# Optimization experiments

Hardware: AMD Instinct MI355X
Metric: run time of the kernel (lower is better)

## Reference

```python
import jax, jax.numpy as jnp
import numpy as np

B, T, H, Dk = 2, 2048, 8, 64
D = H * Dk
MAX_TIMESCALE = 10000.0
MIN_TIMESCALE = 2.0


def sinusoid_position_encoding(seq_len, hidden):
    # Non-causal symmetric relative positions: length 2*seq_len.
    freqs = np.arange(0, hidden, MIN_TIMESCALE)
    inv_freq = MAX_TIMESCALE ** (-freqs / hidden)
    pos_seq = np.arange(seq_len, -seq_len, -1.0)  # [2T]
    sinusoid = np.einsum('i,j->ij', pos_seq, inv_freq)  # [2T, hidden/2]
    pe = np.concatenate([np.sin(sinusoid), np.cos(sinusoid)], axis=-1)
    return jnp.asarray(pe, dtype=jnp.float32)  # [2T, hidden]


def rel_shift(logits):
    # Transformer-XL shift (general, non-causal): [b,h,t,2t] -> [b,h,t,t]
    b, h, t, total = logits.shape  # total == 2t
    x = logits.reshape(b, h, total, t)[:, :, 1:, :]
    x = x.reshape(b, h, t, total - 1)
    return x[..., :t]


def setup_inputs() -> dict:
    key = jax.random.key(0)
    ks = jax.random.split(key, 14)
    s = 1.0 / np.sqrt(D).astype(np.float32)  # VarianceScaling(1.0)-like
    return {
        'query': jax.random.normal(ks[0], (B, T, D), jnp.float32),
        'key_in': jax.random.normal(ks[1], (B, T, D), jnp.float32),
        'value': jax.random.normal(ks[2], (B, T, D), jnp.float32),
        'Wq': jax.random.normal(ks[3], (D, H * Dk), jnp.float32) * s,
        'bq': jnp.zeros((H * Dk,), jnp.float32),
        'Wk': jax.random.normal(ks[4], (D, H * Dk), jnp.float32) * s,
        'bk': jnp.zeros((H * Dk,), jnp.float32),
        'Wv': jax.random.normal(ks[5], (D, H * Dk), jnp.float32) * s,
        'bv': jnp.zeros((H * Dk,), jnp.float32),
        'Wr': jax.random.normal(ks[6], (D, D), jnp.float32) * s,
        'content_bias': jax.random.normal(ks[7], (H, Dk), jnp.float32) * 0.02,
        'relative_bias': jax.random.normal(ks[8], (H, Dk), jnp.float32) * 0.02,
        'Wo': jax.random.normal(ks[9], (H * Dk, D), jnp.float32) * s,
        'bo': jnp.zeros((D,), jnp.float32),
    }


def reference(query, key_in, value, Wq, bq, Wk, bk, Wv, bv, Wr,
              content_bias, relative_bias, Wo, bo):
    q = (query @ Wq + bq).reshape(B, T, H, Dk)
    k = (key_in @ Wk + bk).reshape(B, T, H, Dk)
    v = (value @ Wv + bv).reshape(B, T, H, Dk)

    # Content logits with learned per-head content bias.
    content_logits = jnp.einsum('bthd,bThd->bhtT', q + content_bias, k)

    # Relative-position keys: sinusoid encodings projected (no bias).
    pos = sinusoid_position_encoding(T, D)          # [2T, D]
    rel_k = (pos @ Wr).reshape(2 * T, H, Dk)        # [2T, H, Dk]
    relative_logits = jnp.einsum('bthd,Thd->bhtT', q + relative_bias, rel_k)
    relative_logits = rel_shift(relative_logits)    # [B,H,T,T]

    attn_logits = (content_logits + relative_logits) / np.sqrt(Dk).astype(np.float32)
    attn_weights = jax.nn.softmax(attn_logits)      # [B,H,T,T]

    attn = jnp.einsum('bhtT,bThd->bthd', attn_weights, v)
    attn_vec = attn.reshape(B, T, H * Dk)
    return attn_vec @ Wo + bo
```

## Files before the change

kernel.cpp:

```cpp
#include <hip/hip_runtime.h>
#include <math.h>

#define BB 2
#define TT 2048
#define HH 8
#define DK 64
#define DD 512
#define MM (BB * TT)
#define WSZ (128 * 4096)

typedef unsigned int u32;
typedef unsigned short u16;
typedef __bf16 bf16x8 __attribute__((ext_vector_type(8)));
typedef float f32x4 __attribute__((ext_vector_type(4)));

union frag_u { bf16x8 f; u16 u[8]; u32 w[4]; };

__device__ __forceinline__ void split2(float x, u16& h, u16& l) {
    u32 u = __float_as_uint(x);
    u32 hi = (u + 0x7fffu + ((u >> 16) & 1u)) >> 16;
    float hif = __uint_as_float(hi << 16);
    float lof = x - hif;
    u32 ul = __float_as_uint(lof);
    u32 lo = (ul + 0x7fffu + ((ul >> 16) & 1u)) >> 16;
    h = (u16)hi; l = (u16)lo;
}
__device__ __forceinline__ u32 split_pack(float x) {
    u16 h, l; split2(x, h, l);
    return ((u32)h << 16) | (u32)l;
}
__device__ __forceinline__ u16 bf16_rne(float x) {
    u32 u = __float_as_uint(x);
    return (u16)((u + 0x7fffu + ((u >> 16) & 1u)) >> 16);
}

__device__ __forceinline__ void load_lds16(const void* g, void* l) {
    __builtin_amdgcn_global_load_lds(
        (const __attribute__((address_space(1))) void*)g,
        (__attribute__((address_space(3))) void*)l, 16, 0, 0);
}

__device__ __forceinline__ void pack_granule(const float* xs, u16* dt, int g) {
    u32 hw[4], lw[4];
#pragma unroll
    for (int e = 0; e < 4; e++) {
        u16 h0, l0, h1, l1;
        split2(xs[2 * e], h0, l0);
        split2(xs[2 * e + 1], h1, l1);
        hw[e] = (u32)h0 | ((u32)h1 << 16);
        lw[e] = (u32)l0 | ((u32)l1 << 16);
    }
    *(uint4*)(dt + g * 8)        = make_uint4(hw[0], hw[1], hw[2], hw[3]);
    *(uint4*)(dt + 2048 + g * 8) = make_uint4(lw[0], lw[1], lw[2], lw[3]);
}

__device__ __forceinline__ void prepack_a_body(
    const float* __restrict__ src, u16* __restrict__ dst, int bid, int tid) {
    const int r = tid >> 3, f = tid & 7;
    const float* p = src + ((size_t)(bid >> 3) * 32 + r) * 512
                         + (size_t)(bid & 7) * 64 + f * 8;
    float4 a  = *(const float4*)p;
    float4 b4 = *(const float4*)(p + 4);
    float xs[8] = {a.x, a.y, a.z, a.w, b4.x, b4.y, b4.z, b4.w};
    const int s = f >> 2, kq = f & 3, nt = r >> 4, n = r & 15;
    const int g = nt * 128 + n * 8 + ((4 * s + kq + 5 * n) & 7);
    pack_granule(xs, dst + (size_t)bid * 4096, g);
}

__global__ __launch_bounds__(256) void prepack_all_kernel(
    const float* __restrict__ W0, const float* __restrict__ W1,
    const float* __restrict__ W2, const float* __restrict__ W3,
    const float* __restrict__ W4, u16* __restrict__ dstW,
    u16* __restrict__ dstPe,
    const float* __restrict__ sq, const float* __restrict__ sk,
    const float* __restrict__ sv, u16* __restrict__ dq,
    u16* __restrict__ dk, u16* __restrict__ dv) {
    __shared__ float tw[64][36];
    const int tid = threadIdx.x;
    if (blockIdx.x < 640) {
        const int bid = blockIdx.x;
        const int widx = bid >> 7, loc = bid & 127;
        const int nb2 = loc >> 3, kb = loc & 7;
        const float* Wsrc = widx == 0 ? W0 : widx == 1 ? W1 : widx == 2 ? W2
                          : widx == 3 ? W3 : W4;
        const int kl = tid >> 2, gr = tid & 3;
        const float* p = Wsrc + (size_t)(kb * 64 + kl) * 512 + nb2 * 32 + gr * 8;
        float4 a  = *(const float4*)p;
        float4 b4 = *(const float4*)(p + 4);
        *(float4*)&tw[kl][gr * 8]     = a;
        *(float4*)&tw[kl][gr * 8 + 4] = b4;
        __syncthreads();
        const int n5 = tid >> 3, f = tid & 7, s = f >> 2, kq = f & 3;
        float xs[8];
#pragma unroll
        for (int e = 0; e < 8; e++) xs[e] = tw[s * 32 + kq * 8 + e][n5];
        const int n = n5 & 15, nt = n5 >> 4;
        const int g = nt * 128 + n * 8 + ((4 * s + kq + 5 * n) & 7);
        pack_granule(xs, dstW + (size_t)bid * 4096, g);
    } else if (blockIdx.x < 1664) {
        const int bid = blockIdx.x - 640;
        const int r = tid >> 3, f = tid & 7;
        const int m  = (bid >> 3) * 32 + r;
        const int c0 = (bid & 7) * 64 + f * 8;
        float xs[8];
#pragma unroll
        for (int e = 0; e < 8; e++) {
            int col = c0 + e;
            int j = col & 255;
            double inv_freq = exp((double)(-2 * j) * (9.210340371976184 / 512.0));
            double ang = (double)(TT - m) * inv_freq;
            xs[e] = (col < 256) ? (float)sin(ang) : (float)cos(ang);
        }
        const int s = f >> 2, kq = f & 3, nt = r >> 4, n = r & 15;
        const int g = nt * 128 + n * 8 + ((4 * s + kq + 5 * n) & 7);
        pack_granule(xs, dstPe + (size_t)bid * 4096, g);
    } else {
        const int bid = blockIdx.x - 1664;
        const int sel = bid >> 10, sub = bid & 1023;
        const float* s = sel == 0 ? sq : sel == 1 ? sk : sv;
        u16* d = sel == 0 ? dq : sel == 1 ? dk : dv;
        prepack_a_body(s, d, sub, tid);
    }
}

__device__ __forceinline__ void gemm_full(
    const u16* __restrict__ Apk, const u16* __restrict__ Wpk,
    const float* __restrict__ bias, float* __restrict__ C,
    u16* __restrict__ Ppk, const float* __restrict__ dotv,
    float* __restrict__ dotout, int EPI, int bx, int tid) {
    __shared__ __align__(16) u16 Stage[2][16384];

    const int w = tid >> 6, lane = tid & 63, quad = lane >> 4, c = lane & 15;
    const int mp = bx & 63, nb = bx >> 6;
    const int mq = w >> 1, nq = w & 1;

    auto stage_async = [&](int kb, int half) {
        const u16* s = (w < 2)
            ? Apk + (size_t)((2 * mp + w) * 8 + kb) * 4096
            : Wpk + (size_t)((2 * nb + (w & 1)) * 8 + kb) * 4096;
        const u16* g = s + lane * 8;
        u16* d = Stage[half] + w * 4096;
#pragma unroll
        for (int u2 = 0; u2 < 8; u2++)
            load_lds16(g + u2 * 512, d + u2 * 512);
    };

    stage_async(0, 0);

    f32x4 acc[2][2];
#pragma unroll
    for (int mh = 0; mh < 2; mh++)
#pragma unroll
        for (int nh = 0; nh < 2; nh++) acc[mh][nh] = (f32x4){0.f, 0.f, 0.f, 0.f};

    for (int kb = 0; kb < 8; kb++) {
        const int half = kb & 1;
        __syncthreads();
        if (kb < 7) stage_async(kb + 1, 1 - half);
        const u16* Ab = Stage[half] + mq * 4096;
        const u16* Wb = Stage[half] + 8192 + nq * 4096;
#pragma unroll
        for (int s = 0; s < 2; s++) {
            bf16x8 ah[2], al[2], wh[2], wl[2];
#pragma unroll
            for (int t = 0; t < 2; t++) {
                int g = (t << 7) + (c << 3) + (((s << 2) + quad + 5 * c) & 7);
                ah[t] = *(const bf16x8*)(Ab + g * 8);
                al[t] = *(const bf16x8*)(Ab + 2048 + g * 8);
                wh[t] = *(const bf16x8*)(Wb + g * 8);
                wl[t] = *(const bf16x8*)(Wb + 2048 + g * 8);
            }
#pragma unroll
            for (int mh = 0; mh < 2; mh++)
#pragma unroll
                for (int nh = 0; nh < 2; nh++) {
                    acc[mh][nh] = __builtin_amdgcn_mfma_f32_16x16x32_bf16(
                        ah[mh], wh[nh], acc[mh][nh], 0, 0, 0);
                    acc[mh][nh] = __builtin_amdgcn_mfma_f32_16x16x32_bf16(
                        ah[mh], wl[nh], acc[mh][nh], 0, 0, 0);
                    acc[mh][nh] = __builtin_amdgcn_mfma_f32_16x16x32_bf16(
                        al[mh], wh[nh], acc[mh][nh], 0, 0, 0);
                }
        }
    }

    const int n0 = nb * 64 + nq * 32;
    float bv0 = bias ? bias[n0 + c] : 0.f;
    float bv1 = bias ? bias[n0 + 16 + c] : 0.f;

    if (EPI == 0) {
        const int m0 = mp * 64 + mq * 32;
#pragma unroll
        for (int mh = 0; mh < 2; mh++)
#pragma unroll
            for (int r = 0; r < 4; r++) {
                size_t row = (size_t)(m0 + mh * 16 + quad * 4 + r) * 512;
                C[row + n0 + c]      = acc[mh][0][r] + bv0;
                C[row + n0 + 16 + c] = acc[mh][1][r] + bv1;
            }
        return;
    }

    __syncthreads();
    float (*Cl)[68] = (float (*)[68])Stage;
    {
        const int rbase = mq * 32;
#pragma unroll
        for (int mh = 0; mh < 2; mh++)
#pragma unroll
            for (int r = 0; r < 4; r++) {
                int row = rbase + mh * 16 + quad * 4 + r;
                Cl[row][nq * 32 + c]      = acc[mh][0][r] + bv0;
                Cl[row][nq * 32 + 16 + c] = acc[mh][1][r] + bv1;
            }
    }
    __syncthreads();

    if (EPI == 2) {
        const int b = mp >> 5, jt0 = (mp & 31) * 2;
        const int d = tid >> 2, kq = tid & 3;
        const int n = d & 15;
        const int g = (d >> 4) * 64 + n * 4 + ((kq + (n >> 1)) & 3);
#pragma unroll
        for (int ht = 0; ht < 2; ht++) {
            float xs[8];
#pragma unroll
            for (int e = 0; e < 8; e++) xs[e] = Cl[ht * 32 + kq * 8 + e][d];
            u16* dt = Ppk + (size_t)(b * 512 + nb * 64 + jt0 + ht) * 4096;
            pack_granule(xs, dt, g);
        }
        return;
    }

    {
        const float scl = (EPI == 4) ? 1.0f : 0.125f;
        const int rr = tid >> 3, f = tid & 7;
        const int s = f >> 2, kq = f & 3, nt = rr >> 4, n = rr & 15;
        const int g = nt * 128 + n * 8 + ((4 * s + kq + 5 * n) & 7);
#pragma unroll
        for (int ht = 0; ht < 2; ht++) {
            float xs[8];
#pragma unroll
            for (int e = 0; e < 8; e++) xs[e] = Cl[ht * 32 + rr][f * 8 + e] * scl;
            size_t tidx = (EPI == 1)
                ? (size_t)((mp >> 5) * 512 + nb * 64 + (mp & 31) * 2 + ht)
                : (EPI == 3)
                ? (size_t)(nb * 128 + mp * 2 + ht)
                : (size_t)((mp * 2 + ht) * 8 + nb);
            pack_granule(xs, Ppk + tidx * 4096, g);
        }
    }
    if (EPI != 4 && tid < 64) {
        const float* dv = dotv + nb * 64;
        const float* rowp = Cl[tid];
        float sacc = 0.f;
#pragma unroll
        for (int d = 0; d < 64; d++) sacc += dv[d] * rowp[d];
        int m = mp * 64 + tid;
        if (EPI == 1) {
            int b = m >> 11, t = m & 2047;
            dotout[((size_t)nb * BB + b) * TT + t] = sacc * 0.125f - 8.0f;
        } else {
            dotout[(size_t)nb * 4096 + m] = sacc * 0.125f;
        }
    }
}

__global__ __launch_bounds__(256, 2) void gemm_mfma_kernel(
    const u16* __restrict__ Apk, const u16* __restrict__ Wpk,
    const float* __restrict__ bias, float* __restrict__ C) {
    gemm_full(Apk, Wpk, bias, C, nullptr, nullptr, nullptr, 0,
              blockIdx.x, threadIdx.x);
}

__global__ __launch_bounds__(256, 2) void gemm_relk_kernel(
    const u16* __restrict__ Apk, const u16* __restrict__ Wpk,
    const float* __restrict__ rb, u16* __restrict__ Rpk,
    float* __restrict__ rbrk) {
    gemm_full(Apk, Wpk, nullptr, nullptr, Rpk, rb, rbrk, 3,
              blockIdx.x, threadIdx.x);
}

__global__ __launch_bounds__(256, 2) void gemm3_mfma_kernel(
    const u16* __restrict__ Aq, const u16* __restrict__ Ak,
    const u16* __restrict__ Av, const u16* __restrict__ Wpk,
    const float* __restrict__ bq, const float* __restrict__ bk,
    const float* __restrict__ bv, const float* __restrict__ cb,
    u16* __restrict__ Qpk, u16* __restrict__ Kpk, u16* __restrict__ Vpk,
    float* __restrict__ cbk) {
    const int widx = blockIdx.x >> 9, bx = blockIdx.x & 511;
    const u16* A = widx == 0 ? Aq : widx == 1 ? Ak : Av;
    const u16* W = Wpk + (size_t)widx * WSZ;
    const float* bias = widx == 0 ? bq : widx == 1 ? bk : bv;
    u16* P = widx == 0 ? Qpk : widx == 1 ? Kpk : Vpk;
    const int EPI = widx == 0 ? 4 : widx;
    gemm_full(A, W, bias, nullptr, P, widx == 1 ? cb : nullptr,
              widx == 1 ? cbk : nullptr, EPI, bx, threadIdx.x);
}

__global__ __launch_bounds__(128, 2) void attn_mfma_kernel(
    const u16* __restrict__ Qpk, const u16* __restrict__ Kpk,
    const u16* __restrict__ Vpk, const u16* __restrict__ Rpk,
    const float* __restrict__ cbk, const float* __restrict__ rbrk,
    u16* __restrict__ Aout) {
    __shared__ float Ring[2 * 3 * 1120];
    __shared__ __align__(16) u16 Pbuf[2 * 1280];

    const int tid = threadIdx.x;
    const int w = tid >> 6, lane = tid & 63, quad = lane >> 4, c = lane & 15;
    const int bx = blockIdx.x;
    const int h = bx & 7, b = (bx >> 3) & 1, it = bx >> 4;
    const int i0 = it * 32;

    frag_u qh[2][2], ql[2][2];
    {
        const u16* Qt = Qpk + (size_t)((b * 64 + it) * 8 + h) * 4096;
#pragma unroll
        for (int rg = 0; rg < 2; rg++)
#pragma unroll
            for (int s = 0; s < 2; s++) {
                int g = (rg << 7) + (c << 3) + (((s << 2) + quad + 5 * c) & 7);
                qh[rg][s].f = *(const bf16x8*)(Qt + g * 8);
                ql[rg][s].f = *(const bf16x8*)(Qt + 2048 + g * 8);
            }
    }

    frag_u onesf;
#pragma unroll
    for (int j2 = 0; j2 < 8; j2++) onesf.u[j2] = 0x3f80u;

    const u16* Ktiles  = Kpk + (size_t)(b * HH + h) * 64 * 4096;
    const u16* Vtiles  = Vpk + (size_t)(b * HH + h) * 64 * 4096;
    const u16* Rchunks = Rpk + (size_t)h * 128 * 4096;
    const float* rbrk_h = rbrk + (size_t)h * (2 * TT);
    const float* cbk_h  = cbk + ((size_t)h * BB + b) * TT;

    auto read_kr = [&](const u16* reg, int nt, int s, bf16x8& fh, bf16x8& fl) {
        int g = (nt << 7) + (c << 3) + (((s << 2) + quad + 5 * c) & 7);
        fh = *(const bf16x8*)(reg + g * 8);
        fl = *(const bf16x8*)(reg + 2048 + g * 8);
    };
    auto read_v = [&](const u16* Vb, int ntd, bf16x8& fh, bf16x8& fl) {
        int g = ntd * 64 + c * 4 + ((quad + (c >> 1)) & 3);
        fh = *(const bf16x8*)(Vb + g * 8);
        fl = *(const bf16x8*)(Vb + 2048 + g * 8);
    };

    auto produce = [&](int cidx) {
        const u16* Rc = Rchunks + (size_t)cidx * 4096;
        float* ringw = Ring + (w * 3 + cidx % 3) * 1120;
#pragma unroll
        for (int ntp = 0; ntp < 2; ntp++) {
            f32x4 a0 = {0.f, 0.f, 0.f, 0.f};
            f32x4 a1 = {0.f, 0.f, 0.f, 0.f};
#pragma unroll
            for (int s = 0; s < 2; s++) {
                int g = (ntp << 7) + (c << 3) + (((s << 2) + quad + 5 * c) & 7);
                bf16x8 fh = *(const bf16x8*)(Rc + g * 8);
                bf16x8 fl = *(const bf16x8*)(Rc + 2048 + g * 8);
                a0 = __builtin_amdgcn_mfma_f32_16x16x32_bf16(qh[0][s].f, fh, a0, 0, 0, 0);
                a0 = __builtin_amdgcn_mfma_f32_16x16x32_bf16(qh[0][s].f, fl, a0, 0, 0, 0);
                a0 = __builtin_amdgcn_mfma_f32_16x16x32_bf16(ql[0][s].f, fh, a0, 0, 0, 0);
                a1 = __builtin_amdgcn_mfma_f32_16x16x32_bf16(qh[1][s].f, fh, a1, 0, 0, 0);
                a1 = __builtin_amdgcn_mfma_f32_16x16x32_bf16(qh[1][s].f, fl, a1, 0, 0, 0);
                a1 = __builtin_amdgcn_mfma_f32_16x16x32_bf16(ql[1][s].f, fh, a1, 0, 0, 0);
            }
            float rbv = rbrk_h[cidx * 32 + ntp * 16 + c];
            int mpos = ntp * 16 + c;
#pragma unroll
            for (int r = 0; r < 4; r++)
                ringw[(quad * 4 + r) * 35 + mpos] = a0[r] + rbv;
#pragma unroll
            for (int r = 0; r < 4; r++)
                ringw[(16 + quad * 4 + r) * 35 + mpos] = a1[r] + rbv;
        }
    };

    const int base = TT - i0 + 1024 * w;
    const int F = (base >> 5) - 1;
    produce(F);
    produce(F + 1);

    f32x4 o[2][4];
    f32x4 acc_l[2];
#pragma unroll
    for (int rg = 0; rg < 2; rg++) {
        acc_l[rg] = (f32x4){0.f, 0.f, 0.f, 0.f};
#pragma unroll
        for (int nt = 0; nt < 4; nt++) o[rg][nt] = (f32x4){0.f, 0.f, 0.f, 0.f};
    }

    for (int t = 0; t < 32; t++) {
        const int j0 = 1024 * w + 32 * t;
        const u16* Kb = Ktiles + (size_t)(w * 32 + t) * 4096;
        const u16* Vb = Vtiles + (size_t)(w * 32 + t) * 4096;

        bf16x8 vfh[4], vfl[4];
#pragma unroll
        for (int ntd = 0; ntd < 4; ntd++) read_v(Vb, ntd, vfh[ntd], vfl[ntd]);

        int cnext = F + t + 2;
        if (cnext < 128) produce(cnext);

        const int slo = (F + t) % 3;
        const int shi = (slo == 2) ? 0 : slo + 1;
        const int off_lo = (w * 3 + slo) * 1120;
        const int off_hi = (w * 3 + shi) * 1120;
        float cbv0 = cbk_h[j0 + c];
        float cbv1 = cbk_h[j0 + 16 + c];
        float sv[2][2][4];
#pragma unroll
        for (int nt = 0; nt < 2; nt++) {
            f32x4 sc0 = {0.f, 0.f, 0.f, 0.f};
            f32x4 sc1 = {0.f, 0.f, 0.f, 0.f};
            bf16x8 fh0, fl0, fh1, fl1;
            read_kr(Kb, nt, 0, fh0, fl0);
            read_kr(Kb, nt, 1, fh1, fl1);
            __builtin_amdgcn_s_setprio(1);
            sc0 = __builtin_amdgcn_mfma_f32_16x16x32_bf16(qh[0][0].f, fh0, sc0, 0, 0, 0);
            sc0 = __builtin_amdgcn_mfma_f32_16x16x32_bf16(qh[0][0].f, fl0, sc0, 0, 0, 0);
            sc0 = __builtin_amdgcn_mfma_f32_16x16x32_bf16(ql[0][0].f, fh0, sc0, 0, 0, 0);
            sc0 = __builtin_amdgcn_mfma_f32_16x16x32_bf16(qh[0][1].f, fh1, sc0, 0, 0, 0);
            sc0 = __builtin_amdgcn_mfma_f32_16x16x32_bf16(qh[0][1].f, fl1, sc0, 0, 0, 0);
            sc0 = __builtin_amdgcn_mfma_f32_16x16x32_bf16(ql[0][1].f, fh1, sc0, 0, 0, 0);
            sc1 = __builtin_amdgcn_mfma_f32_16x16x32_bf16(qh[1][0].f, fh0, sc1, 0, 0, 0);
            sc1 = __builtin_amdgcn_mfma_f32_16x16x32_bf16(qh[1][0].f, fl0, sc1, 0, 0, 0);
            sc1 = __builtin_amdgcn_mfma_f32_16x16x32_bf16(ql[1][0].f, fh0, sc1, 0, 0, 0);
            sc1 = __builtin_amdgcn_mfma_f32_16x16x32_bf16(qh[1][1].f, fh1, sc1, 0, 0, 0);
            sc1 = __builtin_amdgcn_mfma_f32_16x16x32_bf16(qh[1][1].f, fl1, sc1, 0, 0, 0);
            sc1 = __builtin_amdgcn_mfma_f32_16x16x32_bf16(ql[1][1].f, fh1, sc1, 0, 0, 0);
            __builtin_amdgcn_s_setprio(0);
            float cbv = nt ? cbv1 : cbv0;
#pragma unroll
            for (int r = 0; r < 4; r++) {
                int row16 = quad * 4 + r;
                int rel0 = nt * 16 + c - row16 + 32;
                float rv0 = Ring[((rel0 >= 32) ? off_hi : off_lo)
                                 + row16 * 35 + (rel0 & 31)];
                sv[0][nt][r] = sc0[r] + rv0 + cbv;
                int rel1 = rel0 - 16;
                float rv1 = Ring[((rel1 >= 32) ? off_hi : off_lo)
                                 + (16 + row16) * 35 + (rel1 & 31)];
                sv[1][nt][r] = sc1[r] + rv1 + cbv;
            }
        }

#pragma unroll
        for (int rg = 0; rg < 2; rg++)
#pragma unroll
            for (int r = 0; r < 4; r++) {
                u16* pb = Pbuf + w * 1280 + (16 * rg + quad * 4 + r) * 40;
                pb[c]      = bf16_rne(__expf(sv[rg][0][r]));
                pb[16 + c] = bf16_rne(__expf(sv[rg][1][r]));
            }

        frag_u ph[2];
#pragma unroll
        for (int rg = 0; rg < 2; rg++) {
            const u16* pb = Pbuf + w * 1280 + (16 * rg + c) * 40 + quad * 8;
            *(uint4*)&ph[rg] = *(const uint4*)pb;
        }
        __builtin_amdgcn_s_setprio(1);
#pragma unroll
        for (int ntd = 0; ntd < 4; ntd++) {
            o[0][ntd] = __builtin_amdgcn_mfma_f32_16x16x32_bf16(ph[0].f, vfh[ntd], o[0][ntd], 0, 0, 0);
            o[0][ntd] = __builtin_amdgcn_mfma_f32_16x16x32_bf16(ph[0].f, vfl[ntd], o[0][ntd], 0, 0, 0);
            o[1][ntd] = __builtin_amdgcn_mfma_f32_16x16x32_bf16(ph[1].f, vfh[ntd], o[1][ntd], 0, 0, 0);
            o[1][ntd] = __builtin_amdgcn_mfma_f32_16x16x32_bf16(ph[1].f, vfl[ntd], o[1][ntd], 0, 0, 0);
        }
        acc_l[0] = __builtin_amdgcn_mfma_f32_16x16x32_bf16(ph[0].f, onesf.f, acc_l[0], 0, 0, 0);
        acc_l[1] = __builtin_amdgcn_mfma_f32_16x16x32_bf16(ph[1].f, onesf.f, acc_l[1], 0, 0, 0);
        __builtin_amdgcn_s_setprio(0);
    }

    float* scr = Ring + 3360;
    if (w == 1) {
#pragma unroll
        for (int rg = 0; rg < 2; rg++) {
#pragma unroll
            for (int nt = 0; nt < 4; nt++)
#pragma unroll
                for (int r = 0; r < 4; r++)
                    scr[(16 * rg + quad * 4 + r) * 65 + nt * 16 + c] = o[rg][nt][r];
            if (c == 0) {
#pragma unroll
                for (int r = 0; r < 4; r++)
                    scr[2080 + 16 * rg + quad * 4 + r] = acc_l[rg][r];
            }
        }
    }
    __syncthreads();
    float* Lp = Ring;
    if (w == 0) {
#pragma unroll
        for (int rg = 0; rg < 2; rg++)
#pragma unroll
            for (int r = 0; r < 4; r++) {
                int row16 = quad * 4 + r;
                int row32 = 16 * rg + row16;
                float invl = 1.0f / (acc_l[rg][r] + scr[2080 + row32]);
#pragma unroll
                for (int nt = 0; nt < 4; nt++)
                    Lp[row32 * 68 + nt * 16 + c] =
                        (o[rg][nt][r] + scr[row32 * 65 + nt * 16 + c]) * invl;
            }
    }
    __syncthreads();
    u16* dt = Aout + (size_t)((b * 64 + it) * 8 + h) * 4096;
#pragma unroll
    for (int pass = 0; pass < 2; pass++) {
        int idx = pass * 128 + tid;
        int rr = idx >> 3, f = idx & 7;
        float xs[8];
#pragma unroll
        for (int e = 0; e < 8; e++) xs[e] = Lp[rr * 68 + f * 8 + e];
        int s = f >> 2, kq = f & 3, nt2 = rr >> 4, n = rr & 15;
        int g = nt2 * 128 + n * 8 + ((4 * s + kq + 5 * n) & 7);
        pack_granule(xs, dt, g);
    }
}

extern "C" void kernel_launch(void* const* d_in, const int* in_sizes, int n_in,
                              void* d_out, int out_size, void* d_ws, size_t ws_size,
                              hipStream_t stream) {
    const float* query  = (const float*)d_in[0];
    const float* key_in = (const float*)d_in[1];
    const float* value  = (const float*)d_in[2];
    const float* Wq = (const float*)d_in[3];
    const float* bq = (const float*)d_in[4];
    const float* Wk = (const float*)d_in[5];
    const float* bk = (const float*)d_in[6];
    const float* Wv = (const float*)d_in[7];
    const float* bv = (const float*)d_in[8];
    const float* Wr = (const float*)d_in[9];
    const float* cb = (const float*)d_in[10];
    const float* rb = (const float*)d_in[11];
    const float* Wo = (const float*)d_in[12];
    const float* bo = (const float*)d_in[13];
    float* out = (float*)d_out;

    float* ws = (float*)d_ws;
    const size_t SL = (size_t)MM * DD;
    u16*   PePk = (u16*)ws;
    u16*   Qpk  = (u16*)ws;
    u16*   Kpk  = (u16*)(ws + 1 * SL);
    u16*   Vpk  = (u16*)(ws + 2 * SL);
    u16*   Rpk  = (u16*)(ws + 3 * SL);
    u16*   s4   = (u16*)(ws + 4 * SL);
    u16*   s5   = (u16*)(ws + 5 * SL);
    u16*   s6   = (u16*)(ws + 6 * SL);
    u16*   Wpk  = (u16*)(ws + 7 * SL);
    float* cbk  = ws + 7 * SL + 1310720;
    float* rbrk = cbk + BB * TT * HH;

    prepack_all_kernel<<<4736, 256, 0, stream>>>(
        Wq, Wk, Wv, Wr, Wo, Wpk, PePk,
        query, key_in, value, s6, s5, s4);

    gemm_relk_kernel<<<512, 256, 0, stream>>>(PePk, Wpk + 3 * WSZ, rb, Rpk, rbrk);

    gemm3_mfma_kernel<<<1536, 256, 0, stream>>>(s6, s5, s4, Wpk, bq, bk, bv,
                                                cb, Qpk, Kpk, Vpk, cbk);

    attn_mfma_kernel<<<BB * HH * (TT / 32), 128, 0, stream>>>(
        Qpk, Kpk, Vpk, Rpk, cbk, rbrk, s4);

    gemm_mfma_kernel<<<512, 256, 0, stream>>>(s4, Wpk + 4 * WSZ, bo, out);
}
```

Before: 243.2 us.

## Load GEMM MFMA fragments directly from global instead of LDS double-buffering

Result: slower. 265.0 us (+9.0%).

```diff
diff --git a/kernel.cpp b/kernel.cpp
--- a/kernel.cpp
+++ b/kernel.cpp
@@ -25,19 +25,9 @@
     u32 lo = (ul + 0x7fffu + ((ul >> 16) & 1u)) >> 16;
     h = (u16)hi; l = (u16)lo;
 }
-__device__ __forceinline__ u32 split_pack(float x) {
-    u16 h, l; split2(x, h, l);
-    return ((u32)h << 16) | (u32)l;
-}
 __device__ __forceinline__ u16 bf16_rne(float x) {
     u32 u = __float_as_uint(x);
     return (u16)((u + 0x7fffu + ((u >> 16) & 1u)) >> 16);
-}
-
-__device__ __forceinline__ void load_lds16(const void* g, void* l) {
-    __builtin_amdgcn_global_load_lds(
-        (const __attribute__((address_space(1))) void*)g,
-        (__attribute__((address_space(3))) void*)l, 16, 0, 0);
 }
 
 __device__ __forceinline__ void pack_granule(const float* xs, u16* dt, int g) {
@@ -128,24 +118,14 @@
     const float* __restrict__ bias, float* __restrict__ C,
     u16* __restrict__ Ppk, const float* __restrict__ dotv,
     float* __restrict__ dotout, int EPI, int bx, int tid) {
-    __shared__ __align__(16) u16 Stage[2][16384];
+    __shared__ float Cl[64][68];
 
     const int w = tid >> 6, lane = tid & 63, quad = lane >> 4, c = lane & 15;
     const int mp = bx & 63, nb = bx >> 6;
     const int mq = w >> 1, nq = w & 1;
 
-    auto stage_async = [&](int kb, int half) {
-        const u16* s = (w < 2)
-            ? Apk + (size_t)((2 * mp + w) * 8 + kb) * 4096
-            : Wpk + (size_t)((2 * nb + (w & 1)) * 8 + kb) * 4096;
-        const u16* g = s + lane * 8;
-        u16* d = Stage[half] + w * 4096;
-#pragma unroll
-        for (int u2 = 0; u2 < 8; u2++)
-            load_lds16(g + u2 * 512, d + u2 * 512);
-    };
-
-    stage_async(0, 0);
+    const u16* Abase = Apk + (size_t)((2 * mp + mq) * 8) * 4096;
+    const u16* Wbase = Wpk + (size_t)((2 * nb + nq) * 8) * 4096;
 
     f32x4 acc[2][2];
 #pragma unroll
@@ -153,12 +133,10 @@
 #pragma unroll
         for (int nh = 0; nh < 2; nh++) acc[mh][nh] = (f32x4){0.f, 0.f, 0.f, 0.f};
 
+#pragma unroll
     for (int kb = 0; kb < 8; kb++) {
-        const int half = kb & 1;
-        __syncthreads();
-        if (kb < 7) stage_async(kb + 1, 1 - half);
-        const u16* Ab = Stage[half] + mq * 4096;
-        const u16* Wb = Stage[half] + 8192 + nq * 4096;
+        const u16* Ab = Abase + (size_t)kb * 4096;
+        const u16* Wb = Wbase + (size_t)kb * 4096;
 #pragma unroll
         for (int s = 0; s < 2; s++) {
             bf16x8 ah[2], al[2], wh[2], wl[2];
@@ -170,6 +148,7 @@
                 wh[t] = *(const bf16x8*)(Wb + g * 8);
                 wl[t] = *(const bf16x8*)(Wb + 2048 + g * 8);
             }
+            __builtin_amdgcn_s_setprio(1);
 #pragma unroll
             for (int mh = 0; mh < 2; mh++)
 #pragma unroll
@@ -181,6 +160,7 @@
                     acc[mh][nh] = __builtin_amdgcn_mfma_f32_16x16x32_bf16(
                         al[mh], wh[nh], acc[mh][nh], 0, 0, 0);
                 }
+            __builtin_amdgcn_s_setprio(0);
         }
     }
 
@@ -201,8 +181,6 @@
         return;
     }
 
-    __syncthreads();
-    float (*Cl)[68] = (float (*)[68])Stage;
     {
         const int rbase = mq * 32;
 #pragma unroll
@@ -266,14 +244,14 @@
     }
 }
 
-__global__ __launch_bounds__(256, 2) void gemm_mfma_kernel(
+__global__ __launch_bounds__(256, 3) void gemm_mfma_kernel(
     const u16* __restrict__ Apk, const u16* __restrict__ Wpk,
     const float* __restrict__ bias, float* __restrict__ C) {
     gemm_full(Apk, Wpk, bias, C, nullptr, nullptr, nullptr, 0,
               blockIdx.x, threadIdx.x);
 }
 
-__global__ __launch_bounds__(256, 2) void gemm_relk_kernel(
+__global__ __launch_bounds__(256, 3) void gemm_relk_kernel(
     const u16* __restrict__ Apk, const u16* __restrict__ Wpk,
     const float* __restrict__ rb, u16* __restrict__ Rpk,
     float* __restrict__ rbrk) {
@@ -281,7 +259,7 @@
               blockIdx.x, threadIdx.x);
 }
 
-__global__ __launch_bounds__(256, 2) void gemm3_mfma_kernel(
+__global__ __launch_bounds__(256, 3) void gemm3_mfma_kernel(
     const u16* __restrict__ Aq, const u16* __restrict__ Ak,
     const u16* __restrict__ Av, const u16* __restrict__ Wpk,
     const float* __restrict__ bq, const float* __restrict__ bk,
```
